# Optimization experiments

Measured on AMD Instinct MI355X. Metric: run time of the kernel, lower is better.

## Reference

```python
import jax, jax.numpy as jnp
import numpy as np
import math

H = 14
W = 14
MU_MAX = math.sqrt((H / 2) ** 2 + (W / 2) ** 2)
EPS = 1e-6
LN_EPS = 1e-5


def _distance_sq():
    fy = np.fft.fftfreq(H) * H
    fx = np.fft.rfftfreq(W) * W
    d = fy[:, None] ** 2 + fx[None, :] ** 2  # (H, W//2+1)
    return jnp.asarray(d[None, None], dtype=jnp.float32)  # (1,1,H,W//2+1)


def setup_inputs() -> dict:
    key = jax.random.key(0)
    k0, k1, k2 = jax.random.split(key, 3)
    B, C, HID = 256, 768, 192  # hidden = max(768//4, 8)
    return {
        "x": jax.random.normal(k0, (B, 197, C), jnp.float32),
        "ln_gamma": jnp.ones((C,), jnp.float32),
        "ln_beta": jnp.zeros((C,), jnp.float32),
        "w1": jax.random.normal(k1, (C, HID), jnp.float32) * 0.02,
        "b1": jnp.zeros((HID,), jnp.float32),
        "w2": jax.random.normal(k2, (HID, 2), jnp.float32) * 0.02,
        "b2": jnp.zeros((2,), jnp.float32),
        "residual_scale": jnp.asarray(1e-4, jnp.float32),
    }


def reference(x, ln_gamma, ln_beta, w1, b1, w2, b2, residual_scale):
    b, _, c = x.shape
    cls_tok = x[:, :1]          # (B,1,C)
    xs = x[:, 1:]               # (B,196,C) raw spatial tokens
    # LayerNorm (biased variance, eps=1e-5 like torch default)
    mu_ln = xs.mean(-1, keepdims=True)
    var_ln = xs.var(-1, keepdims=True)
    xn = (xs - mu_ln) / jnp.sqrt(var_ln + LN_EPS) * ln_gamma + ln_beta
    # to (B,C,H,W) grid
    xg = xn.transpose(0, 2, 1).reshape(b, c, H, W)
    xm = xg.mean((-2, -1), keepdims=True)
    spec = jnp.fft.rfft2(xg - xm, norm='ortho')  # (B,C,H,W//2+1) complex
    energy = jnp.log1p(jnp.abs(spec)).mean((-2, -1))  # (B,C)
    hdn = jax.nn.gelu(energy @ w1 + b1, approximate=False)
    out2 = hdn @ w2 + b2  # (B,2)
    mu = jnp.maximum(MU_MAX * jax.nn.sigmoid(out2[:, 0]), 1.0).reshape(b, 1, 1, 1)
    sigma = jnp.maximum(jax.nn.softplus(out2[:, 1]), 0.1).reshape(b, 1, 1, 1)
    mask = jnp.exp(-_distance_sq() / (2.0 * mu ** 2 * sigma + EPS))
    filtered = jnp.fft.irfft2(spec * mask, s=(H, W), norm='ortho') + xm
    toks = filtered.reshape(b, c, H * W).transpose(0, 2, 1)  # (B,196,C)
    delta = toks - xn
    return jnp.concatenate([cls_tok, xs + residual_scale * delta], axis=1)
```

## Files before the change

### kernel.cpp

```cpp
#include <hip/hip_runtime.h>
#include <math.h>

#define NB    256
#define NTOKP 197
#define NTOK  196
#define NC    768
#define NHID  192
#define NH    14
#define NVF   8
#define CHT   64
#define NTILE 12

constexpr float CT14[14] = {
    1.0f, 0.9009688679024191f, 0.6234898018587336f, 0.22252093395631445f,
    -0.22252093395631434f, -0.6234898018587335f, -0.9009688679024191f, -1.0f,
    -0.9009688679024191f, -0.6234898018587335f, -0.22252093395631434f,
    0.22252093395631445f, 0.6234898018587336f, 0.9009688679024191f};
constexpr float ST14[14] = {
    0.0f, 0.4338837391175581f, 0.7818314824680298f, 0.9749279121818236f,
    0.9749279121818236f, 0.7818314824680299f, 0.43388373911755823f, 0.0f,
    -0.43388373911755823f, -0.7818314824680299f, -0.9749279121818236f,
    -0.9749279121818236f, -0.7818314824680298f, -0.4338837391175581f};

__device__ __forceinline__ unsigned int pack_bf2(float a, float b) {
  return (__float_as_uint(a) >> 16) | (__float_as_uint(b) & 0xFFFF0000u);
}

__global__ __launch_bounds__(256) void k_stats(const float* __restrict__ x,
                                               float2* __restrict__ msv) {
  int row = blockIdx.x * 4 + (threadIdx.x >> 6);
  int lane = threadIdx.x & 63;
  if (row >= NB * NTOK) return;
  int b = row / NTOK, t = row - b * NTOK;
  const float4* p = (const float4*)(x + ((size_t)b * NTOKP + 1 + t) * NC);
  float s = 0.f, ss = 0.f;
#pragma unroll
  for (int k = 0; k < 3; ++k) {
    float4 v = p[lane + k * 64];
    s += v.x + v.y + v.z + v.w;
    ss += v.x * v.x + v.y * v.y + v.z * v.z + v.w * v.w;
  }
#pragma unroll
  for (int off = 32; off; off >>= 1) {
    s += __shfl_down(s, off);
    ss += __shfl_down(ss, off);
  }
  if (lane == 0) {
    float m = s * (1.f / NC);
    float var = ss * (1.f / NC) - m * m;
    msv[row] = make_float2(m, rsqrtf(var + 1e-5f));
  }
}

__global__ __launch_bounds__(256) void k_fwd(const float* __restrict__ x,
                                             const float* __restrict__ gamma,
                                             const float* __restrict__ beta,
                                             const float2* __restrict__ msv,
                                             float* __restrict__ energy,
                                             float* __restrict__ xmv) {
  __shared__ unsigned int A[NH * NVF * CHT];
  __shared__ float2 ms[NTOK];
  __shared__ float esum[256];
  int b = blockIdx.y, c0 = blockIdx.x * CHT, tid = threadIdx.x;
  int c = tid & 63, w = tid >> 6;

  for (int k = tid; k < NTOK; k += 256) ms[k] = msv[b * NTOK + k];
  float g = gamma[c0 + c], be = beta[c0 + c];
  __syncthreads();

#pragma unroll 1
  for (int i = w; i < NH; i += 4) {
    const float* xr = x + ((size_t)b * NTOKP + 1 + i * NH) * NC + c0 + c;
    float xn_[NH];
#pragma unroll
    for (int j = 0; j < NH; ++j) {
      float2 m = ms[i * NH + j];
      xn_[j] = (xr[(size_t)j * NC] - m.x) * m.y * g + be;
    }
    float ar[NVF] = {}, ai[NVF] = {};
#pragma unroll
    for (int j = 0; j < NH; ++j) {
#pragma unroll
      for (int v = 0; v < NVF; ++v) {
        ar[v] = fmaf(xn_[j], CT14[(v * j) % 14], ar[v]);
        ai[v] = fmaf(-xn_[j], ST14[(v * j) % 14], ai[v]);
      }
    }
#pragma unroll
    for (int v = 0; v < NVF; ++v) A[(i * NVF + v) * CHT + c] = pack_bf2(ar[v], ai[v]);
  }
  __syncthreads();

  float part = 0.f, xml = 0.f;
#pragma unroll 1
  for (int vv = 0; vv < 2; ++vv) {
    int v = w * 2 + vv;
    const unsigned int* Ac = A + v * CHT + c;
    float sr[NH], si[NH];
#pragma unroll
    for (int u = 0; u < NH; ++u) { sr[u] = 0.f; si[u] = 0.f; }
#pragma unroll
    for (int i = 0; i < NH; ++i) {
      unsigned int p = Ac[i * NVF * CHT];
      float ar = __uint_as_float(p << 16);
      float ai = __uint_as_float(p & 0xFFFF0000u);
#pragma unroll
      for (int u = 0; u < NH; ++u) {
        int idx = (u * i) % 14;
        sr[u] = fmaf(ar, CT14[idx], fmaf(ai, ST14[idx], sr[u]));
        si[u] = fmaf(ai, CT14[idx], fmaf(-ar, ST14[idx], si[u]));
      }
    }
#pragma unroll
    for (int u = 0; u < NH; ++u) {
      float m2 = sr[u] * sr[u] + si[u] * si[u];
      part += __logf(1.f + __builtin_amdgcn_sqrtf(m2) * (1.f / 14.f));
    }
    if (w == 0 && vv == 0) {
      xml = sr[0] * (1.f / 196.f);
      part -= __logf(1.f + fabsf(sr[0]) * (1.f / 14.f));
    }
  }
  esum[tid] = part;
  __syncthreads();
  if (w == 0) {
    float e = esum[c] + esum[c + 64] + esum[c + 128] + esum[c + 192];
    energy[b * NC + c0 + c] = e * (1.f / 112.f);
    xmv[b * NC + c0 + c] = xml;
  }
}

__global__ __launch_bounds__(256) void k_mlp(const float* __restrict__ energy,
                                             const float* __restrict__ w1,
                                             const float* __restrict__ b1,
                                             const float* __restrict__ w2,
                                             const float* __restrict__ b2,
                                             float* __restrict__ m2s) {
  __shared__ float e[NC];
  __shared__ float hd[NHID];
  int b = blockIdx.x, tid = threadIdx.x;
  for (int k = tid; k < NC; k += 256) e[k] = energy[b * NC + k];
  __syncthreads();
  if (tid < NHID) {
    float acc = b1[tid];
    for (int cc = 0; cc < NC; ++cc) acc = fmaf(e[cc], w1[cc * NHID + tid], acc);
    hd[tid] = 0.5f * acc * (1.f + erff(acc * 0.70710678118654752f));
  }
  __syncthreads();
  if (tid < 64) {
    float p0 = 0.f, p1 = 0.f;
#pragma unroll
    for (int k = 0; k < 3; ++k) {
      float hv = hd[tid + k * 64];
      p0 = fmaf(hv, w2[2 * (tid + k * 64)], p0);
      p1 = fmaf(hv, w2[2 * (tid + k * 64) + 1], p1);
    }
#pragma unroll
    for (int off = 32; off; off >>= 1) {
      p0 += __shfl_down(p0, off);
      p1 += __shfl_down(p1, off);
    }
    if (tid == 0) {
      float o0 = p0 + b2[0], o1 = p1 + b2[1];
      float muv = 9.899494936611665f / (1.f + expf(-o0));
      muv = fmaxf(muv, 1.f);
      float sp = (o1 > 20.f) ? o1 : log1pf(expf(o1));
      float sg = fmaxf(sp, 0.1f);
      m2s[b] = 2.f * muv * muv * sg + 1e-6f;
    }
  }
}

__global__ __launch_bounds__(256) void k_inv(const float* __restrict__ x,
                                             const float* __restrict__ gamma,
                                             const float* __restrict__ beta,
                                             const float2* __restrict__ msv,
                                             const float* __restrict__ xmv,
                                             const float* __restrict__ m2s,
                                             const float* __restrict__ rscale,
                                             float* __restrict__ out) {
  __shared__ unsigned int T[NH * 7 * CHT];
  __shared__ float2 ms[NTOK];
  __shared__ float wexp[NH];
  __shared__ float kc[NH];
  int b = blockIdx.y, c0 = blockIdx.x * CHT, tid = threadIdx.x;
  int c = tid & 63, w = tid >> 6;
  float rs = rscale[0];

  for (int k = tid; k < NTOK; k += 256) ms[k] = msv[b * NTOK + k];
  if (tid < CHT) {
    size_t idx = (size_t)b * NTOKP * NC + c0 + tid;
    out[idx] = x[idx];
  }
  float msb = m2s[b];
  if (tid < NH) {
    int f = (tid <= 7) ? tid : 14 - tid;
    wexp[tid] = __expf(-(float)(f * f) / msb);
  }
  __syncthreads();
  if (tid < NH) {
    float s = 0.f;
#pragma unroll
    for (int k = 0; k < NH; ++k)
      s = fmaf(wexp[k], __cosf((float)(k * tid) * 0.44879895051282760f), s);
    kc[tid] = s * (1.f / 14.f);
  }
  float g = gamma[c0 + c], be = beta[c0 + c];
  float xm = xmv[b * NC + c0 + c];
  __syncthreads();

  float kr[NH];
#pragma unroll
  for (int d = 0; d < NH; ++d) kr[d] = kc[d];

#pragma unroll 1
  for (int i = w; i < NH; i += 4) {
    const float* xr = x + ((size_t)b * NTOKP + 1 + i * NH) * NC + c0 + c;
    float xnc[NH];
#pragma unroll
    for (int j = 0; j < NH; ++j) {
      float2 m = ms[i * NH + j];
      xnc[j] = (xr[(size_t)j * NC] - m.x) * m.y * g + be - xm;
    }
#pragma unroll
    for (int jp = 0; jp < 7; ++jp) {
      float y0 = 0.f, y1 = 0.f;
#pragma unroll
      for (int j = 0; j < NH; ++j) {
        y0 = fmaf(xnc[j], kr[(2 * jp - j + 28) % 14], y0);
        y1 = fmaf(xnc[j], kr[(2 * jp + 1 - j + 28) % 14], y1);
      }
      T[(i * 7 + jp) * CHT + c] = pack_bf2(y0, y1);
    }
  }
  __syncthreads();

#pragma unroll 1
  for (int jq = w; jq < NH; jq += 4) {
    int jp = jq >> 1, hi = jq & 1;
    float y[NH];
#pragma unroll
    for (int i = 0; i < NH; ++i) {
      unsigned int p = T[(i * 7 + jp) * CHT + c];
      y[i] = __uint_as_float((p >> (16 * hi)) << 16);
    }
    const float* xr = x + ((size_t)b * NTOKP + 1 + jq) * NC + c0 + c;
    float* outr = out + ((size_t)b * NTOKP + 1 + jq) * NC + c0 + c;
#pragma unroll
    for (int ii = 0; ii < NH; ++ii) {
      float z = 0.f;
#pragma unroll
      for (int i = 0; i < NH; ++i) z = fmaf(y[i], kr[(ii - i + 28) % 14], z);
      float xv = xr[(size_t)ii * NH * NC];
      float2 m = ms[ii * NH + jq];
      float xn = (xv - m.x) * m.y * g + be;
      outr[(size_t)ii * NH * NC] = xv + rs * (z + xm - xn);
    }
  }
}

extern "C" void kernel_launch(void* const* d_in, const int* in_sizes, int n_in,
                              void* d_out, int out_size, void* d_ws, size_t ws_size,
                              hipStream_t stream) {
  (void)in_sizes; (void)n_in; (void)out_size; (void)ws_size;
  const float* x      = (const float*)d_in[0];
  const float* gamma  = (const float*)d_in[1];
  const float* beta   = (const float*)d_in[2];
  const float* w1     = (const float*)d_in[3];
  const float* b1     = (const float*)d_in[4];
  const float* w2     = (const float*)d_in[5];
  const float* b2     = (const float*)d_in[6];
  const float* rscale = (const float*)d_in[7];
  float* out = (float*)d_out;

  float* wsf    = (float*)d_ws;
  float2* msv   = (float2*)wsf;
  float* energy = wsf + 100352;
  float* xmv    = wsf + 296960;
  float* m2s    = wsf + 493568;

  k_stats<<<(NB * NTOK + 3) / 4, 256, 0, stream>>>(x, msv);
  k_fwd<<<dim3(NTILE, NB), 256, 0, stream>>>(x, gamma, beta, msv, energy, xmv);
  k_mlp<<<NB, 256, 0, stream>>>(energy, w1, b1, w2, b2, m2s);
  k_inv<<<dim3(NTILE, NB), 256, 0, stream>>>(x, gamma, beta, msv, xmv, m2s,
                                             rscale, out);
}
```

Measured before the change: 170.9 us.

## Reuse fp16 normalized tile in LDS instead of re-reading x in inverse pass

The inverse kernel now keeps the normalized tokens in LDS as fp16 pairs and rebuilds the raw x values from them, so the second global read of x in the output stage goes away. The forward pass switches its intermediate storage from bf16 to fp16 and splits the 14-point column DFT into even and odd 7-point halves, which cuts the FMA count. The per-channel mean (xm) buffer is dropped, since filtering xn directly is equivalent when the DC mask is 1. Smaller changes replace __cosf with a constant table and unroll the MLP loop. Rebuilding x from fp16 values adds rounding error to the passthrough term of the output, which risks the accuracy tolerance.

```diff
diff --git a/kernel.cpp b/kernel.cpp
--- a/kernel.cpp
+++ b/kernel.cpp
@@ -1,4 +1,5 @@
 #include <hip/hip_runtime.h>
+#include <hip/hip_fp16.h>
 #include <math.h>
 
 #define NB    256
@@ -21,9 +22,20 @@
     0.9749279121818236f, 0.7818314824680299f, 0.43388373911755823f, 0.0f,
     -0.43388373911755823f, -0.7818314824680299f, -0.9749279121818236f,
     -0.9749279121818236f, -0.7818314824680298f, -0.4338837391175581f};
-
-__device__ __forceinline__ unsigned int pack_bf2(float a, float b) {
-  return (__float_as_uint(a) >> 16) | (__float_as_uint(b) & 0xFFFF0000u);
+constexpr float C7[7] = {1.0f, 0.6234898018587336f, -0.22252093395631434f,
+                         -0.9009688679024191f, -0.9009688679024191f,
+                         -0.22252093395631434f, 0.6234898018587336f};
+constexpr float S7[7] = {0.0f, 0.7818314824680298f, 0.9749279121818236f,
+                         0.4338837391175581f, -0.4338837391175581f,
+                         -0.9749279121818236f, -0.7818314824680298f};
+
+__device__ __forceinline__ unsigned int pack_h2(float a, float b) {
+  __half2 h = __floats2half2_rn(a, b);
+  return *(unsigned int*)&h;
+}
+__device__ __forceinline__ float2 unpack_h2(unsigned int p) {
+  __half2 h = *(__half2*)&p;
+  return __half22float2(h);
 }
 
 __global__ __launch_bounds__(256) void k_stats(const float* __restrict__ x,
@@ -56,8 +68,7 @@
                                              const float* __restrict__ gamma,
                                              const float* __restrict__ beta,
                                              const float2* __restrict__ msv,
-                                             float* __restrict__ energy,
-                                             float* __restrict__ xmv) {
+                                             float* __restrict__ energy) {
   __shared__ unsigned int A[NH * NVF * CHT];
   __shared__ float2 ms[NTOK];
   __shared__ float esum[256];
@@ -87,38 +98,44 @@
       }
     }
 #pragma unroll
-    for (int v = 0; v < NVF; ++v) A[(i * NVF + v) * CHT + c] = pack_bf2(ar[v], ai[v]);
-  }
-  __syncthreads();
-
-  float part = 0.f, xml = 0.f;
+    for (int v = 0; v < NVF; ++v) A[(i * NVF + v) * CHT + c] = pack_h2(ar[v], ai[v]);
+  }
+  __syncthreads();
+
+  float part = 0.f;
 #pragma unroll 1
   for (int vv = 0; vv < 2; ++vv) {
     int v = w * 2 + vv;
     const unsigned int* Ac = A + v * CHT + c;
-    float sr[NH], si[NH];
-#pragma unroll
-    for (int u = 0; u < NH; ++u) { sr[u] = 0.f; si[u] = 0.f; }
-#pragma unroll
-    for (int i = 0; i < NH; ++i) {
-      unsigned int p = Ac[i * NVF * CHT];
-      float ar = __uint_as_float(p << 16);
-      float ai = __uint_as_float(p & 0xFFFF0000u);
-#pragma unroll
-      for (int u = 0; u < NH; ++u) {
-        int idx = (u * i) % 14;
-        sr[u] = fmaf(ar, CT14[idx], fmaf(ai, ST14[idx], sr[u]));
-        si[u] = fmaf(ai, CT14[idx], fmaf(-ar, ST14[idx], si[u]));
+    float er[7], ei[7], orr[7], oii[7];
+#pragma unroll
+    for (int k = 0; k < 7; ++k) { er[k] = 0.f; ei[k] = 0.f; orr[k] = 0.f; oii[k] = 0.f; }
+#pragma unroll
+    for (int m = 0; m < 7; ++m) {
+      float2 ae = unpack_h2(Ac[(2 * m) * NVF * CHT]);
+      float2 ao = unpack_h2(Ac[(2 * m + 1) * NVF * CHT]);
+#pragma unroll
+      for (int k = 0; k < 7; ++k) {
+        int t = (k * m) % 7;
+        er[k] = fmaf(ae.x, C7[t], fmaf(ae.y, S7[t], er[k]));
+        ei[k] = fmaf(ae.y, C7[t], fmaf(-ae.x, S7[t], ei[k]));
+        orr[k] = fmaf(ao.x, C7[t], fmaf(ao.y, S7[t], orr[k]));
+        oii[k] = fmaf(ao.y, C7[t], fmaf(-ao.x, S7[t], oii[k]));
       }
     }
 #pragma unroll
     for (int u = 0; u < NH; ++u) {
-      float m2 = sr[u] * sr[u] + si[u] * si[u];
-      part += __logf(1.f + __builtin_amdgcn_sqrtf(m2) * (1.f / 14.f));
-    }
-    if (w == 0 && vv == 0) {
-      xml = sr[0] * (1.f / 196.f);
-      part -= __logf(1.f + fabsf(sr[0]) * (1.f / 14.f));
+      int k = u % 7;
+      float tr = fmaf(orr[k], CT14[u], oii[k] * ST14[u]);
+      float ti = fmaf(oii[k], CT14[u], -orr[k] * ST14[u]);
+      float sr = er[k] + tr, si = ei[k] + ti;
+      float m2 = fmaf(sr, sr, si * si);
+      float lg = __logf(1.f + __builtin_amdgcn_sqrtf(m2) * (1.f / 14.f));
+      if (u == 0) {
+        if (v != 0) part += lg;
+      } else {
+        part += lg;
+      }
     }
   }
   esum[tid] = part;
@@ -126,7 +143,6 @@
   if (w == 0) {
     float e = esum[c] + esum[c + 64] + esum[c + 128] + esum[c + 192];
     energy[b * NC + c0 + c] = e * (1.f / 112.f);
-    xmv[b * NC + c0 + c] = xml;
   }
 }
 
@@ -143,6 +159,7 @@
   __syncthreads();
   if (tid < NHID) {
     float acc = b1[tid];
+#pragma unroll 4
     for (int cc = 0; cc < NC; ++cc) acc = fmaf(e[cc], w1[cc * NHID + tid], acc);
     hd[tid] = 0.5f * acc * (1.f + erff(acc * 0.70710678118654752f));
   }
@@ -175,19 +192,24 @@
                                              const float* __restrict__ gamma,
                                              const float* __restrict__ beta,
                                              const float2* __restrict__ msv,
-                                             const float* __restrict__ xmv,
                                              const float* __restrict__ m2s,
                                              const float* __restrict__ rscale,
                                              float* __restrict__ out) {
+  __shared__ unsigned int X[NH * 7 * CHT];
   __shared__ unsigned int T[NH * 7 * CHT];
   __shared__ float2 ms[NTOK];
+  __shared__ float rr[NTOK];
   __shared__ float wexp[NH];
   __shared__ float kc[NH];
   int b = blockIdx.y, c0 = blockIdx.x * CHT, tid = threadIdx.x;
   int c = tid & 63, w = tid >> 6;
   float rs = rscale[0];
 
-  for (int k = tid; k < NTOK; k += 256) ms[k] = msv[b * NTOK + k];
+  for (int k = tid; k < NTOK; k += 256) {
+    float2 m = msv[b * NTOK + k];
+    ms[k] = m;
+    rr[k] = 1.f / m.y;
+  }
   if (tid < CHT) {
     size_t idx = (size_t)b * NTOKP * NC + c0 + tid;
     out[idx] = x[idx];
@@ -201,12 +223,11 @@
   if (tid < NH) {
     float s = 0.f;
 #pragma unroll
-    for (int k = 0; k < NH; ++k)
-      s = fmaf(wexp[k], __cosf((float)(k * tid) * 0.44879895051282760f), s);
+    for (int k = 0; k < NH; ++k) s = fmaf(wexp[k], CT14[(k * tid) % 14], s);
     kc[tid] = s * (1.f / 14.f);
   }
   float g = gamma[c0 + c], be = beta[c0 + c];
-  float xm = xmv[b * NC + c0 + c];
+  float rg = 1.f / g;
   __syncthreads();
 
   float kr[NH];
@@ -216,21 +237,24 @@
 #pragma unroll 1
   for (int i = w; i < NH; i += 4) {
     const float* xr = x + ((size_t)b * NTOKP + 1 + i * NH) * NC + c0 + c;
-    float xnc[NH];
+    float xn_[NH];
 #pragma unroll
     for (int j = 0; j < NH; ++j) {
       float2 m = ms[i * NH + j];
-      xnc[j] = (xr[(size_t)j * NC] - m.x) * m.y * g + be - xm;
-    }
+      xn_[j] = (xr[(size_t)j * NC] - m.x) * m.y * g + be;
+    }
+#pragma unroll
+    for (int k = 0; k < 7; ++k)
+      X[(i * 7 + k) * CHT + c] = pack_h2(xn_[2 * k], xn_[2 * k + 1]);
 #pragma unroll
     for (int jp = 0; jp < 7; ++jp) {
       float y0 = 0.f, y1 = 0.f;
 #pragma unroll
       for (int j = 0; j < NH; ++j) {
-        y0 = fmaf(xnc[j], kr[(2 * jp - j + 28) % 14], y0);
-        y1 = fmaf(xnc[j], kr[(2 * jp + 1 - j + 28) % 14], y1);
+        y0 = fmaf(xn_[j], kr[(2 * jp - j + 28) % 14], y0);
+        y1 = fmaf(xn_[j], kr[(2 * jp + 1 - j + 28) % 14], y1);
       }
-      T[(i * 7 + jp) * CHT + c] = pack_bf2(y0, y1);
+      T[(i * 7 + jp) * CHT + c] = pack_h2(y0, y1);
     }
   }
   __syncthreads();
@@ -241,20 +265,20 @@
     float y[NH];
 #pragma unroll
     for (int i = 0; i < NH; ++i) {
-      unsigned int p = T[(i * 7 + jp) * CHT + c];
-      y[i] = __uint_as_float((p >> (16 * hi)) << 16);
-    }
-    const float* xr = x + ((size_t)b * NTOKP + 1 + jq) * NC + c0 + c;
+      float2 v = unpack_h2(T[(i * 7 + jp) * CHT + c]);
+      y[i] = hi ? v.y : v.x;
+    }
     float* outr = out + ((size_t)b * NTOKP + 1 + jq) * NC + c0 + c;
 #pragma unroll
     for (int ii = 0; ii < NH; ++ii) {
       float z = 0.f;
 #pragma unroll
       for (int i = 0; i < NH; ++i) z = fmaf(y[i], kr[(ii - i + 28) % 14], z);
-      float xv = xr[(size_t)ii * NH * NC];
-      float2 m = ms[ii * NH + jq];
-      float xn = (xv - m.x) * m.y * g + be;
-      outr[(size_t)ii * NH * NC] = xv + rs * (z + xm - xn);
+      float2 v = unpack_h2(X[(ii * 7 + jp) * CHT + c]);
+      float xnv = hi ? v.y : v.x;
+      int t = ii * NH + jq;
+      float xv = fmaf((xnv - be) * rg, rr[t], ms[t].x);
+      outr[(size_t)ii * NH * NC] = xv + rs * (z - xnv);
     }
   }
 }
@@ -276,12 +300,11 @@
   float* wsf    = (float*)d_ws;
   float2* msv   = (float2*)wsf;
   float* energy = wsf + 100352;
-  float* xmv    = wsf + 296960;
-  float* m2s    = wsf + 493568;
+  float* m2s    = wsf + 296960;
 
   k_stats<<<(NB * NTOK + 3) / 4, 256, 0, stream>>>(x, msv);
-  k_fwd<<<dim3(NTILE, NB), 256, 0, stream>>>(x, gamma, beta, msv, energy, xmv);
+  k_fwd<<<dim3(NTILE, NB), 256, 0, stream>>>(x, gamma, beta, msv, energy);
   k_mlp<<<NB, 256, 0, stream>>>(energy, w1, b1, w2, b2, m2s);
-  k_inv<<<dim3(NTILE, NB), 256, 0, stream>>>(x, gamma, beta, msv, xmv, m2s,
-                                             rscale, out);
-}
+  k_inv<<<dim3(NTILE, NB), 256, 0, stream>>>(x, gamma, beta, msv, m2s, rscale,
+                                             out);
+}
```

Result: slower. 191.6 us (+12.1%).

## Batch-parallel MLP with transposed energy, fp16 LDS packing, drop mean pass-through

Applied to the files above, without the earlier changes.

The per-batch MLP kernel, where every block streams all of w1, is split into two kernels. The first assigns one thread per batch element and a few hidden units per block, reading energy stored channel-major so loads are coalesced and w1 values are broadcast across threads. The spatial-mean bookkeeping is removed, relying on the filter's unit DC gain to pass the mean through the inverse transform. Intermediate LDS packing changes from bf16 to fp16, which is more precise but has less range. The runtime cosine in the filter-kernel setup is replaced by a lookup table. The split adds a kernel launch, and the first MLP kernel runs only 48 blocks.

```diff
diff --git a/kernel.cpp b/kernel.cpp
--- a/kernel.cpp
+++ b/kernel.cpp
@@ -1,4 +1,5 @@
 #include <hip/hip_runtime.h>
+#include <hip/hip_fp16.h>
 #include <math.h>
 
 #define NB    256
@@ -10,6 +11,7 @@
 #define NVF   8
 #define CHT   64
 #define NTILE 12
+#define HPB   4
 
 constexpr float CT14[14] = {
     1.0f, 0.9009688679024191f, 0.6234898018587336f, 0.22252093395631445f,
@@ -22,8 +24,13 @@
     -0.43388373911755823f, -0.7818314824680299f, -0.9749279121818236f,
     -0.9749279121818236f, -0.7818314824680298f, -0.4338837391175581f};
 
-__device__ __forceinline__ unsigned int pack_bf2(float a, float b) {
-  return (__float_as_uint(a) >> 16) | (__float_as_uint(b) & 0xFFFF0000u);
+__device__ __forceinline__ unsigned int pack_h2(float a, float b) {
+  __half2 h = __floats2half2_rn(a, b);
+  return *(unsigned int*)&h;
+}
+__device__ __forceinline__ float2 unpack_h2(unsigned int p) {
+  __half2 h = *(__half2*)&p;
+  return __half22float2(h);
 }
 
 __global__ __launch_bounds__(256) void k_stats(const float* __restrict__ x,
@@ -56,8 +63,7 @@
                                              const float* __restrict__ gamma,
                                              const float* __restrict__ beta,
                                              const float2* __restrict__ msv,
-                                             float* __restrict__ energy,
-                                             float* __restrict__ xmv) {
+                                             float* __restrict__ energy_t) {
   __shared__ unsigned int A[NH * NVF * CHT];
   __shared__ float2 ms[NTOK];
   __shared__ float esum[256];
@@ -87,11 +93,11 @@
       }
     }
 #pragma unroll
-    for (int v = 0; v < NVF; ++v) A[(i * NVF + v) * CHT + c] = pack_bf2(ar[v], ai[v]);
-  }
-  __syncthreads();
-
-  float part = 0.f, xml = 0.f;
+    for (int v = 0; v < NVF; ++v) A[(i * NVF + v) * CHT + c] = pack_h2(ar[v], ai[v]);
+  }
+  __syncthreads();
+
+  float part = 0.f;
 #pragma unroll 1
   for (int vv = 0; vv < 2; ++vv) {
     int v = w * 2 + vv;
@@ -101,23 +107,20 @@
     for (int u = 0; u < NH; ++u) { sr[u] = 0.f; si[u] = 0.f; }
 #pragma unroll
     for (int i = 0; i < NH; ++i) {
-      unsigned int p = Ac[i * NVF * CHT];
-      float ar = __uint_as_float(p << 16);
-      float ai = __uint_as_float(p & 0xFFFF0000u);
+      float2 a = unpack_h2(Ac[i * NVF * CHT]);
 #pragma unroll
       for (int u = 0; u < NH; ++u) {
         int idx = (u * i) % 14;
-        sr[u] = fmaf(ar, CT14[idx], fmaf(ai, ST14[idx], sr[u]));
-        si[u] = fmaf(ai, CT14[idx], fmaf(-ar, ST14[idx], si[u]));
+        sr[u] = fmaf(a.x, CT14[idx], fmaf(a.y, ST14[idx], sr[u]));
+        si[u] = fmaf(a.y, CT14[idx], fmaf(-a.x, ST14[idx], si[u]));
       }
     }
 #pragma unroll
     for (int u = 0; u < NH; ++u) {
-      float m2 = sr[u] * sr[u] + si[u] * si[u];
+      float m2 = fmaf(sr[u], sr[u], si[u] * si[u]);
       part += __logf(1.f + __builtin_amdgcn_sqrtf(m2) * (1.f / 14.f));
     }
     if (w == 0 && vv == 0) {
-      xml = sr[0] * (1.f / 196.f);
       part -= __logf(1.f + fabsf(sr[0]) * (1.f / 14.f));
     }
   }
@@ -125,57 +128,55 @@
   __syncthreads();
   if (w == 0) {
     float e = esum[c] + esum[c + 64] + esum[c + 128] + esum[c + 192];
-    energy[b * NC + c0 + c] = e * (1.f / 112.f);
-    xmv[b * NC + c0 + c] = xml;
-  }
-}
-
-__global__ __launch_bounds__(256) void k_mlp(const float* __restrict__ energy,
-                                             const float* __restrict__ w1,
-                                             const float* __restrict__ b1,
-                                             const float* __restrict__ w2,
-                                             const float* __restrict__ b2,
-                                             float* __restrict__ m2s) {
-  __shared__ float e[NC];
-  __shared__ float hd[NHID];
-  int b = blockIdx.x, tid = threadIdx.x;
-  for (int k = tid; k < NC; k += 256) e[k] = energy[b * NC + k];
-  __syncthreads();
-  if (tid < NHID) {
-    float acc = b1[tid];
-    for (int cc = 0; cc < NC; ++cc) acc = fmaf(e[cc], w1[cc * NHID + tid], acc);
-    hd[tid] = 0.5f * acc * (1.f + erff(acc * 0.70710678118654752f));
-  }
-  __syncthreads();
-  if (tid < 64) {
-    float p0 = 0.f, p1 = 0.f;
-#pragma unroll
-    for (int k = 0; k < 3; ++k) {
-      float hv = hd[tid + k * 64];
-      p0 = fmaf(hv, w2[2 * (tid + k * 64)], p0);
-      p1 = fmaf(hv, w2[2 * (tid + k * 64) + 1], p1);
-    }
-#pragma unroll
-    for (int off = 32; off; off >>= 1) {
-      p0 += __shfl_down(p0, off);
-      p1 += __shfl_down(p1, off);
-    }
-    if (tid == 0) {
-      float o0 = p0 + b2[0], o1 = p1 + b2[1];
-      float muv = 9.899494936611665f / (1.f + expf(-o0));
-      muv = fmaxf(muv, 1.f);
-      float sp = (o1 > 20.f) ? o1 : log1pf(expf(o1));
-      float sg = fmaxf(sp, 0.1f);
-      m2s[b] = 2.f * muv * muv * sg + 1e-6f;
-    }
-  }
+    energy_t[(size_t)(c0 + c) * NB + b] = e * (1.f / 112.f);
+  }
+}
+
+__global__ __launch_bounds__(256) void k_mlp1(const float* __restrict__ et,
+                                              const float* __restrict__ w1,
+                                              const float* __restrict__ b1,
+                                              float* __restrict__ hdt) {
+  int h0 = blockIdx.x * HPB;
+  int bb = threadIdx.x;
+  float acc[HPB];
+#pragma unroll
+  for (int k = 0; k < HPB; ++k) acc[k] = b1[h0 + k];
+  for (int cc = 0; cc < NC; ++cc) {
+    float e = et[(size_t)cc * NB + bb];
+#pragma unroll
+    for (int k = 0; k < HPB; ++k)
+      acc[k] = fmaf(e, w1[cc * NHID + h0 + k], acc[k]);
+  }
+#pragma unroll
+  for (int k = 0; k < HPB; ++k) {
+    float a = acc[k];
+    float ge = 0.5f * a * (1.f + erff(a * 0.70710678118654752f));
+    hdt[(size_t)(h0 + k) * NB + bb] = ge;
+  }
+}
+
+__global__ __launch_bounds__(256) void k_mlp2(const float* __restrict__ hdt,
+                                              const float* __restrict__ w2,
+                                              const float* __restrict__ b2,
+                                              float* __restrict__ m2s) {
+  int bb = threadIdx.x;
+  float a0 = b2[0], a1 = b2[1];
+  for (int h = 0; h < NHID; ++h) {
+    float hv = hdt[(size_t)h * NB + bb];
+    a0 = fmaf(hv, w2[2 * h], a0);
+    a1 = fmaf(hv, w2[2 * h + 1], a1);
+  }
+  float muv = 9.899494936611665f / (1.f + expf(-a0));
+  muv = fmaxf(muv, 1.f);
+  float sp = (a1 > 20.f) ? a1 : log1pf(expf(a1));
+  float sg = fmaxf(sp, 0.1f);
+  m2s[bb] = 2.f * muv * muv * sg + 1e-6f;
 }
 
 __global__ __launch_bounds__(256) void k_inv(const float* __restrict__ x,
                                              const float* __restrict__ gamma,
                                              const float* __restrict__ beta,
                                              const float2* __restrict__ msv,
-                                             const float* __restrict__ xmv,
                                              const float* __restrict__ m2s,
                                              const float* __restrict__ rscale,
                                              float* __restrict__ out) {
@@ -201,12 +202,10 @@
   if (tid < NH) {
     float s = 0.f;
 #pragma unroll
-    for (int k = 0; k < NH; ++k)
-      s = fmaf(wexp[k], __cosf((float)(k * tid) * 0.44879895051282760f), s);
+    for (int k = 0; k < NH; ++k) s = fmaf(wexp[k], CT14[(k * tid) % 14], s);
     kc[tid] = s * (1.f / 14.f);
   }
   float g = gamma[c0 + c], be = beta[c0 + c];
-  float xm = xmv[b * NC + c0 + c];
   __syncthreads();
 
   float kr[NH];
@@ -216,21 +215,21 @@
 #pragma unroll 1
   for (int i = w; i < NH; i += 4) {
     const float* xr = x + ((size_t)b * NTOKP + 1 + i * NH) * NC + c0 + c;
-    float xnc[NH];
+    float xn_[NH];
 #pragma unroll
     for (int j = 0; j < NH; ++j) {
       float2 m = ms[i * NH + j];
-      xnc[j] = (xr[(size_t)j * NC] - m.x) * m.y * g + be - xm;
+      xn_[j] = (xr[(size_t)j * NC] - m.x) * m.y * g + be;
     }
 #pragma unroll
     for (int jp = 0; jp < 7; ++jp) {
       float y0 = 0.f, y1 = 0.f;
 #pragma unroll
       for (int j = 0; j < NH; ++j) {
-        y0 = fmaf(xnc[j], kr[(2 * jp - j + 28) % 14], y0);
-        y1 = fmaf(xnc[j], kr[(2 * jp + 1 - j + 28) % 14], y1);
+        y0 = fmaf(xn_[j], kr[(2 * jp - j + 28) % 14], y0);
+        y1 = fmaf(xn_[j], kr[(2 * jp + 1 - j + 28) % 14], y1);
       }
-      T[(i * 7 + jp) * CHT + c] = pack_bf2(y0, y1);
+      T[(i * 7 + jp) * CHT + c] = pack_h2(y0, y1);
     }
   }
   __syncthreads();
@@ -241,8 +240,8 @@
     float y[NH];
 #pragma unroll
     for (int i = 0; i < NH; ++i) {
-      unsigned int p = T[(i * 7 + jp) * CHT + c];
-      y[i] = __uint_as_float((p >> (16 * hi)) << 16);
+      float2 v = unpack_h2(T[(i * 7 + jp) * CHT + c]);
+      y[i] = hi ? v.y : v.x;
     }
     const float* xr = x + ((size_t)b * NTOKP + 1 + jq) * NC + c0 + c;
     float* outr = out + ((size_t)b * NTOKP + 1 + jq) * NC + c0 + c;
@@ -254,7 +253,7 @@
       float xv = xr[(size_t)ii * NH * NC];
       float2 m = ms[ii * NH + jq];
       float xn = (xv - m.x) * m.y * g + be;
-      outr[(size_t)ii * NH * NC] = xv + rs * (z + xm - xn);
+      outr[(size_t)ii * NH * NC] = xv + rs * (z - xn);
     }
   }
 }
@@ -273,15 +272,16 @@
   const float* rscale = (const float*)d_in[7];
   float* out = (float*)d_out;
 
-  float* wsf    = (float*)d_ws;
-  float2* msv   = (float2*)wsf;
-  float* energy = wsf + 100352;
-  float* xmv    = wsf + 296960;
-  float* m2s    = wsf + 493568;
+  char* wsb = (char*)d_ws;
+  float2* msv     = (float2*)(wsb + 0);
+  float* energy_t = (float*)(wsb + 401408);
+  float* hdt      = (float*)(wsb + 1187840);
+  float* m2s      = (float*)(wsb + 1384448);
 
   k_stats<<<(NB * NTOK + 3) / 4, 256, 0, stream>>>(x, msv);
-  k_fwd<<<dim3(NTILE, NB), 256, 0, stream>>>(x, gamma, beta, msv, energy, xmv);
-  k_mlp<<<NB, 256, 0, stream>>>(energy, w1, b1, w2, b2, m2s);
-  k_inv<<<dim3(NTILE, NB), 256, 0, stream>>>(x, gamma, beta, msv, xmv, m2s,
-                                             rscale, out);
-}
+  k_fwd<<<dim3(NTILE, NB), 256, 0, stream>>>(x, gamma, beta, msv, energy_t);
+  k_mlp1<<<NHID / HPB, 256, 0, stream>>>(energy_t, w1, b1, hdt);
+  k_mlp2<<<1, 256, 0, stream>>>(hdt, w2, b2, m2s);
+  k_inv<<<dim3(NTILE, NB), 256, 0, stream>>>(x, gamma, beta, msv, m2s, rscale,
+                                             out);
+}
```

After: 244.4 us. 1.43x slower.
